# Optimization experiments

Measured on AMD Instinct MI355X. Metric: run time of the kernel, lower is better.

## Reference

```python
import jax, jax.numpy as jnp
import numpy as np

T = 1024
H = 256
W = 256
D1 = 512
D2 = 1024


def setup_inputs() -> dict:
    key = jax.random.key(0)
    ks = jax.random.split(key, 8)
    B = 16
    x_true = jax.random.normal(ks[0], (B, H, W), dtype=jnp.float32)
    k_points = 0.25 * jax.random.normal(ks[1], (T, 2), dtype=jnp.float32)
    # torch Linear default init ~ U(-1/sqrt(fan_in), 1/sqrt(fan_in)); scale suffices
    def lin(k, fi, fo):
        s = 1.0 / np.sqrt(fi)
        return jax.random.uniform(k, (fi, fo), jnp.float32, -s, s)
    W1 = lin(ks[2], 2 * T, D1)
    b1 = jnp.zeros((D1,), jnp.float32)
    W2 = lin(ks[3], D1, D2)
    b2 = jnp.zeros((D2,), jnp.float32)
    W3 = lin(ks[4], D2, H * W)
    b3 = jnp.zeros((H * W,), jnp.float32)
    return {"x_true": x_true, "k_points": k_points, "W1": W1, "b1": b1,
            "W2": W2, "b2": b2, "W3": W3, "b3": b3}


def _fourier_sample(x, k_points):
    # phase[t,h,w] = exp(-2pi i (kx[t]*xx[w] + ky[t]*yy[h])) = px[t,w]*py[t,h]
    xx = jnp.linspace(-0.5, 0.5, W)  # (W,)
    yy = jnp.linspace(-0.5, 0.5, H)  # (H,)
    two_pi = 2.0 * jnp.pi
    px = jnp.exp(-1j * two_pi * k_points[:, 0:1] * xx[None, :])  # (T, W) complex
    py = jnp.exp(-1j * two_pi * k_points[:, 1:2] * yy[None, :])  # (T, H) complex
    # samples[b,t] = sum_{h,w} x[b,h,w] * px[t,w] * py[t,h]
    a = jnp.einsum('bhw,tw->bth', x.astype(jnp.complex64), px)  # (B, T, H)
    return jnp.einsum('bth,th->bt', a, py)  # (B, T) complex


def reference(x_true, k_points, W1, b1, W2, b2, W3, b3):
    y = _fourier_sample(x_true, k_points)  # (B, T) complex
    feat = jnp.concatenate([y.real, y.imag], axis=-1)  # (B, 2T)
    h1 = jax.nn.relu(feat @ W1 + b1)
    h2 = jax.nn.relu(h1 @ W2 + b2)
    out = h2 @ W3 + b3
    x_hat = out.reshape(x_true.shape[0], H, W)
    return (x_hat, y, k_points)
```

## Files before the change

### kernel.cpp

```cpp
#include <hip/hip_runtime.h>
#include <hip/hip_bf16.h>
#include <math.h>

#define WS_PB     0u
#define WS_PYRE   262144u
#define WS_PYIM   524288u
#define WS_XB     786432u
#define WS_FEAT   1310720u
#define WS_H1ACC  1343488u
#define WS_H1F    1351680u
#define WS_H2ACC  1359872u
#define WS_H2T    1376256u

#define OUT_Y  1048576

typedef __attribute__((ext_vector_type(8))) short short8;
typedef __attribute__((ext_vector_type(4))) float f32x4;

__device__ inline unsigned short f2bf(float f) {
  __hip_bfloat16 h = __float2bfloat16(f);
  return *reinterpret_cast<unsigned short*>(&h);
}

__global__ void k0_cvt(const float* __restrict__ x, unsigned short* __restrict__ xb) {
  int i = (blockIdx.x * 256 + threadIdx.x) * 4;
  float4 v = *(const float4*)(x + i);
  ushort4 o;
  o.x = f2bf(v.x); o.y = f2bf(v.y); o.z = f2bf(v.z); o.w = f2bf(v.w);
  *(ushort4*)(xb + i) = o;
}

__global__ void k1_trig(const float* __restrict__ kp, unsigned short* __restrict__ Pb,
                        float* __restrict__ pyre, float* __restrict__ pyim) {
  int bid = blockIdx.x, tid = threadIdx.x;
  const float TWO_PI = 6.28318530717958647692f;
  if (bid < 1024) {
    int t = bid, w = tid;
    float kx = kp[2 * t];
    float xx = -0.5f + (float)w * (1.0f / 255.0f);
    float s, c;
    sincosf(TWO_PI * kx * xx, &s, &c);
    Pb[t * 256 + w]          = f2bf(c);
    Pb[(1024 + t) * 256 + w] = f2bf(-s);
  } else {
    int t = bid - 1024, h = tid;
    float ky = kp[2 * t + 1];
    float yy = -0.5f + (float)h * (1.0f / 255.0f);
    float s, c;
    sincosf(TWO_PI * ky * yy, &s, &c);
    pyre[t * 256 + h] = c;
    pyim[t * 256 + h] = -s;
  }
}

#define TPAD 40

__launch_bounds__(256)
__global__ void k23_fused(const unsigned short* __restrict__ Pb,
                          const unsigned short* __restrict__ xb,
                          const float* __restrict__ pyre, const float* __restrict__ pyim,
                          float* __restrict__ feat, float* __restrict__ out_y,
                          float* __restrict__ h1_acc, int ymode) {
  __shared__ unsigned short Alds[64 * TPAD];
  __shared__ unsigned short Xlds[256 * TPAD];
  __shared__ float red[32][4][4];
  int tid = threadIdx.x;
  int b  = blockIdx.y;
  int t0 = blockIdx.x * 32;
  int w = tid >> 6, l = tid & 63;
  int g = l >> 4, c = l & 15;
  const unsigned short* xbase = xb + (size_t)b * 65536;

  f32x4 acc[4][4] = {};

  for (int ks = 0; ks < 8; ++ks) {
    int k0 = ks * 32;
    __syncthreads();
    {
      int row = tid >> 2, seg = tid & 3;
      int trow = (row < 32) ? (t0 + row) : (1024 + t0 + row - 32);
      *(uint4*)(&Alds[row * TPAD + seg * 8]) =
          *(const uint4*)(Pb + (size_t)trow * 256 + k0 + seg * 8);
    }
    {
      const unsigned short* src = xbase + (size_t)tid * 256 + k0;
      unsigned short* dst = &Xlds[tid * TPAD];
      *(uint4*)(dst)      = *(const uint4*)(src);
      *(uint4*)(dst + 8)  = *(const uint4*)(src + 8);
      *(uint4*)(dst + 16) = *(const uint4*)(src + 16);
      *(uint4*)(dst + 24) = *(const uint4*)(src + 24);
    }
    __syncthreads();
    short8 afr[4], bfr[4];
    #pragma unroll
    for (int mf = 0; mf < 4; ++mf)
      afr[mf] = *reinterpret_cast<const short8*>(&Alds[(mf * 16 + c) * TPAD + g * 8]);
    #pragma unroll
    for (int hf = 0; hf < 4; ++hf)
      bfr[hf] = *reinterpret_cast<const short8*>(&Xlds[(w * 64 + hf * 16 + c) * TPAD + g * 8]);
    #pragma unroll
    for (int mf = 0; mf < 4; ++mf)
      #pragma unroll
      for (int hf = 0; hf < 4; ++hf)
        acc[mf][hf] = __builtin_amdgcn_mfma_f32_16x16x32_bf16(afr[mf], bfr[hf], acc[mf][hf], 0, 0, 0);
  }

  float srr[2][4] = {{0}}, sii[2][4] = {{0}}, sri[2][4] = {{0}}, sir[2][4] = {{0}};
  #pragma unroll
  for (int mh = 0; mh < 2; ++mh)
    #pragma unroll
    for (int r = 0; r < 4; ++r) {
      int t = t0 + mh * 16 + g * 4 + r;
      #pragma unroll
      for (int hf = 0; hf < 4; ++hf) {
        int h = w * 64 + hf * 16 + c;
        float cr = pyre[t * 256 + h], ci = pyim[t * 256 + h];
        float vre = acc[mh][hf][r], vim = acc[mh + 2][hf][r];
        srr[mh][r] += vre * cr; sri[mh][r] += vre * ci;
        sir[mh][r] += vim * cr; sii[mh][r] += vim * ci;
      }
    }
  #pragma unroll
  for (int mh = 0; mh < 2; ++mh)
    #pragma unroll
    for (int r = 0; r < 4; ++r) {
      float a0 = srr[mh][r], a1 = sii[mh][r], a2 = sri[mh][r], a3 = sir[mh][r];
      #pragma unroll
      for (int off = 1; off < 16; off <<= 1) {
        a0 += __shfl_xor(a0, off, 64);
        a1 += __shfl_xor(a1, off, 64);
        a2 += __shfl_xor(a2, off, 64);
        a3 += __shfl_xor(a3, off, 64);
      }
      if (c == 0) {
        int tloc = mh * 16 + g * 4 + r;
        red[tloc][w][0] = a0; red[tloc][w][1] = a1;
        red[tloc][w][2] = a2; red[tloc][w][3] = a3;
      }
    }
  __syncthreads();
  if (tid < 32) {
    int t = t0 + tid;
    float yre = 0.f, yim = 0.f;
    #pragma unroll
    for (int ww = 0; ww < 4; ++ww) {
      yre += red[tid][ww][0] - red[tid][ww][1];
      yim += red[tid][ww][2] + red[tid][ww][3];
    }
    feat[b * 2048 + t]        = yre;
    feat[b * 2048 + 1024 + t] = yim;
    if (ymode == 0) {
      out_y[b * 1024 + t] = yre;
    } else {
      out_y[(b * 1024 + t) * 2]     = yre;
      out_y[(b * 1024 + t) * 2 + 1] = yim;
    }
  }
  if (blockIdx.y == 0) h1_acc[blockIdx.x * 256 + tid] = 0.f;
}

__global__ void k4_w1(const float* __restrict__ feat, const float* __restrict__ W1,
                      float* __restrict__ h1_acc) {
  int nt = blockIdx.x & 1, ks = blockIdx.x >> 1;
  int n = nt * 256 + threadIdx.x;
  int k0 = ks * 64;
  float acc[16];
  #pragma unroll
  for (int b = 0; b < 16; ++b) acc[b] = 0.f;
  for (int k = k0; k < k0 + 64; ++k) {
    float w = W1[k * 512 + n];
    #pragma unroll
    for (int b = 0; b < 16; ++b) acc[b] += feat[b * 2048 + k] * w;
  }
  #pragma unroll
  for (int b = 0; b < 16; ++b) atomicAdd(&h1_acc[b * 512 + n], acc[b]);
}

__global__ void k4b_fin(const float* __restrict__ h1_acc, const float* __restrict__ b1,
                        float* __restrict__ h1f, float* __restrict__ h2_acc) {
  int i = blockIdx.x * 256 + threadIdx.x;
  if (i < 8192) {
    int k = i & 511;
    h1f[i] = fmaxf(h1_acc[i] + b1[k], 0.f);
  }
  if (i < 16384) h2_acc[i] = 0.f;
}

__global__ void k5_w2(const float* __restrict__ h1f, const float* __restrict__ W2,
                      float* __restrict__ h2_acc) {
  int nt = blockIdx.x & 3, ks = blockIdx.x >> 2;
  int n = nt * 256 + threadIdx.x;
  int k0 = ks * 32;
  float acc[16];
  #pragma unroll
  for (int b = 0; b < 16; ++b) acc[b] = 0.f;
  for (int k = k0; k < k0 + 32; ++k) {
    float w = W2[k * 1024 + n];
    #pragma unroll
    for (int b = 0; b < 16; ++b) acc[b] += h1f[b * 512 + k] * w;
  }
  #pragma unroll
  for (int b = 0; b < 16; ++b) atomicAdd(&h2_acc[b * 1024 + n], acc[b]);
}

__global__ void k5b_fin(const float* __restrict__ h2_acc, const float* __restrict__ b2,
                        const float* __restrict__ kp, float* __restrict__ h2t,
                        float* __restrict__ out_kp) {
  int i = blockIdx.x * 256 + threadIdx.x;
  if (i < 16384) {
    int k = i >> 4, b = i & 15;
    h2t[i] = fmaxf(h2_acc[b * 1024 + k] + b2[k], 0.f);
  } else {
    int j = i - 16384;
    out_kp[j] = kp[j];
  }
}

__launch_bounds__(512, 1)
__global__ void k6_w3(const float* __restrict__ h2t, const float* __restrict__ W3,
                      const float* __restrict__ b3, float* __restrict__ out) {
  __shared__ float red[256][17];
  int tn = threadIdx.x & 255;
  int kh = threadIdx.x >> 8;
  int n = blockIdx.x * 256 + tn;
  int k0 = kh * 512;
  float acc[16];
  #pragma unroll
  for (int b = 0; b < 16; ++b) acc[b] = 0.f;
  const float* w3p = W3 + (size_t)k0 * 65536 + n;
  const float4* hp = (const float4*)(h2t + k0 * 16);
  #pragma unroll 8
  for (int k = 0; k < 512; ++k) {
    float w = w3p[(size_t)k * 65536];
    float4 h0 = hp[k * 4 + 0];
    float4 h1 = hp[k * 4 + 1];
    float4 h2 = hp[k * 4 + 2];
    float4 h3 = hp[k * 4 + 3];
    acc[0]  += h0.x * w; acc[1]  += h0.y * w; acc[2]  += h0.z * w; acc[3]  += h0.w * w;
    acc[4]  += h1.x * w; acc[5]  += h1.y * w; acc[6]  += h1.z * w; acc[7]  += h1.w * w;
    acc[8]  += h2.x * w; acc[9]  += h2.y * w; acc[10] += h2.z * w; acc[11] += h2.w * w;
    acc[12] += h3.x * w; acc[13] += h3.y * w; acc[14] += h3.z * w; acc[15] += h3.w * w;
  }
  if (kh) {
    #pragma unroll
    for (int b = 0; b < 16; ++b) red[tn][b] = acc[b];
  }
  __syncthreads();
  if (!kh) {
    float bv = b3[n];
    #pragma unroll
    for (int b = 0; b < 16; ++b)
      out[(size_t)b * 65536 + n] = acc[b] + red[tn][b] + bv;
  }
}

extern "C" void kernel_launch(void* const* d_in, const int* in_sizes, int n_in,
                              void* d_out, int out_size, void* d_ws, size_t ws_size,
                              hipStream_t stream) {
  const float* x  = (const float*)d_in[0];
  const float* kp = (const float*)d_in[1];
  const float* W1 = (const float*)d_in[2];
  const float* b1 = (const float*)d_in[3];
  const float* W2 = (const float*)d_in[4];
  const float* b2 = (const float*)d_in[5];
  const float* W3 = (const float*)d_in[6];
  const float* b3 = (const float*)d_in[7];
  float* out = (float*)d_out;
  float* ws  = (float*)d_ws;

  unsigned short* Pb = (unsigned short*)(ws + WS_PB);
  float* pyre   = ws + WS_PYRE;
  float* pyim   = ws + WS_PYIM;
  unsigned short* xb = (unsigned short*)(ws + WS_XB);
  float* feat   = ws + WS_FEAT;
  float* h1_acc = ws + WS_H1ACC;
  float* h1f    = ws + WS_H1F;
  float* h2_acc = ws + WS_H2ACC;
  float* h2t    = ws + WS_H2T;

  int ymode = (out_size == 1048576 + 16384 + 2048) ? 0 : 1;
  float* out_y  = out + OUT_Y;
  float* out_kp = out + (out_size - 2048);

  k0_cvt<<<dim3(1024), dim3(256), 0, stream>>>(x, xb);
  k1_trig<<<dim3(2048), dim3(256), 0, stream>>>(kp, Pb, pyre, pyim);
  k23_fused<<<dim3(32, 16), dim3(256), 0, stream>>>(Pb, xb, pyre, pyim, feat, out_y, h1_acc, ymode);
  k4_w1<<<dim3(64), dim3(256), 0, stream>>>(feat, W1, h1_acc);
  k4b_fin<<<dim3(96), dim3(256), 0, stream>>>(h1_acc, b1, h1f, h2_acc);
  k5_w2<<<dim3(64), dim3(256), 0, stream>>>(h1f, W2, h2_acc);
  k5b_fin<<<dim3(72), dim3(256), 0, stream>>>(h2_acc, b2, kp, h2t, out_kp);
  k6_w3<<<dim3(256), dim3(512), 0, stream>>>(h2t, W3, b3, out);
}
```

Before: 512.4 us.

## Split W3 GEMV over K across blocks with LDS-staged activations and reduction kernel

The final W3 layer now splits the K dimension into four chunks along a second grid dimension, giving 512 blocks of 256 threads instead of 256 blocks of 512. Each thread handles two adjacent output columns through float2 loads, and the h2 activations for its chunk are staged in shared memory. Partial sums go to a workspace buffer, and a separate kernel adds the four partials plus the bias. The aim is more parallelism and better use of memory bandwidth when streaming the 256 MB W3 matrix. The cost is an extra 16 MB of partial-sum traffic and one more kernel launch.

Result: faster. 439.6 us (-14.2%).

```diff
diff --git a/kernel.cpp b/kernel.cpp
--- a/kernel.cpp
+++ b/kernel.cpp
@@ -11,6 +11,7 @@
 #define WS_H1F    1351680u
 #define WS_H2ACC  1359872u
 #define WS_H2T    1376256u
+#define WS_PT     1392640u
 
 #define OUT_Y  1048576
 
@@ -216,42 +217,49 @@
   }
 }
 
-__launch_bounds__(512, 1)
+__launch_bounds__(256, 2)
 __global__ void k6_w3(const float* __restrict__ h2t, const float* __restrict__ W3,
-                      const float* __restrict__ b3, float* __restrict__ out) {
-  __shared__ float red[256][17];
-  int tn = threadIdx.x & 255;
-  int kh = threadIdx.x >> 8;
-  int n = blockIdx.x * 256 + tn;
-  int k0 = kh * 512;
-  float acc[16];
-  #pragma unroll
-  for (int b = 0; b < 16; ++b) acc[b] = 0.f;
+                      float* __restrict__ pt) {
+  __shared__ float hs[256][16];
+  int tid = threadIdx.x;
+  int kc = blockIdx.y;
+  int k0 = kc * 256;
+  int n = blockIdx.x * 512 + tid * 2;
+  {
+    const float4* src = (const float4*)(h2t + (size_t)(k0 + tid) * 16);
+    float4* dst = (float4*)hs[tid];
+    dst[0] = src[0]; dst[1] = src[1]; dst[2] = src[2]; dst[3] = src[3];
+  }
+  __syncthreads();
+  float accx[16] = {}, accy[16] = {};
   const float* w3p = W3 + (size_t)k0 * 65536 + n;
-  const float4* hp = (const float4*)(h2t + k0 * 16);
   #pragma unroll 8
-  for (int k = 0; k < 512; ++k) {
-    float w = w3p[(size_t)k * 65536];
-    float4 h0 = hp[k * 4 + 0];
-    float4 h1 = hp[k * 4 + 1];
-    float4 h2 = hp[k * 4 + 2];
-    float4 h3 = hp[k * 4 + 3];
-    acc[0]  += h0.x * w; acc[1]  += h0.y * w; acc[2]  += h0.z * w; acc[3]  += h0.w * w;
-    acc[4]  += h1.x * w; acc[5]  += h1.y * w; acc[6]  += h1.z * w; acc[7]  += h1.w * w;
-    acc[8]  += h2.x * w; acc[9]  += h2.y * w; acc[10] += h2.z * w; acc[11] += h2.w * w;
-    acc[12] += h3.x * w; acc[13] += h3.y * w; acc[14] += h3.z * w; acc[15] += h3.w * w;
-  }
-  if (kh) {
-    #pragma unroll
-    for (int b = 0; b < 16; ++b) red[tn][b] = acc[b];
-  }
-  __syncthreads();
-  if (!kh) {
-    float bv = b3[n];
-    #pragma unroll
-    for (int b = 0; b < 16; ++b)
-      out[(size_t)b * 65536 + n] = acc[b] + red[tn][b] + bv;
-  }
+  for (int k = 0; k < 256; ++k) {
+    float2 w = *(const float2*)(w3p + (size_t)k * 65536);
+    const float* hr = hs[k];
+    #pragma unroll
+    for (int b = 0; b < 16; ++b) {
+      accx[b] += hr[b] * w.x;
+      accy[b] += hr[b] * w.y;
+    }
+  }
+  float* pb = pt + (size_t)kc * 16 * 65536 + n;
+  #pragma unroll
+  for (int b = 0; b < 16; ++b)
+    *(float2*)(pb + (size_t)b * 65536) = make_float2(accx[b], accy[b]);
+}
+
+__global__ void k6b_red(const float* __restrict__ pt, const float* __restrict__ b3,
+                        float* __restrict__ out) {
+  int i = (blockIdx.x * 256 + threadIdx.x) * 4;
+  int n = i & 65535;
+  float4 s = *(const float4*)(b3 + n);
+  #pragma unroll
+  for (int kc = 0; kc < 4; ++kc) {
+    float4 p = *(const float4*)(pt + (size_t)kc * 1048576 + i);
+    s.x += p.x; s.y += p.y; s.z += p.z; s.w += p.w;
+  }
+  *(float4*)(out + i) = s;
 }
 
 extern "C" void kernel_launch(void* const* d_in, const int* in_sizes, int n_in,
@@ -277,6 +285,7 @@
   float* h1f    = ws + WS_H1F;
   float* h2_acc = ws + WS_H2ACC;
   float* h2t    = ws + WS_H2T;
+  float* pt     = ws + WS_PT;
 
   int ymode = (out_size == 1048576 + 16384 + 2048) ? 0 : 1;
   float* out_y  = out + OUT_Y;
@@ -289,5 +298,6 @@
   k4b_fin<<<dim3(96), dim3(256), 0, stream>>>(h1_acc, b1, h1f, h2_acc);
   k5_w2<<<dim3(64), dim3(256), 0, stream>>>(h1f, W2, h2_acc);
   k5b_fin<<<dim3(72), dim3(256), 0, stream>>>(h2_acc, b2, kp, h2t, out_kp);
-  k6_w3<<<dim3(256), dim3(512), 0, stream>>>(h2t, W3, b3, out);
-}
+  k6_w3<<<dim3(128, 4), dim3(256), 0, stream>>>(h2t, W3, pt);
+  k6b_red<<<dim3(1024), dim3(256), 0, stream>>>(pt, b3, out);
+}
```
